# Optimization experiments

Measured on AMD Instinct MI355X. Metric: run time of the kernel, lower is better.

## Reference

```python
import jax, jax.numpy as jnp
import numpy as np

B, H, W, D, O = 16, 128, 128, 64, 256

def setup_inputs() -> dict:
    key = jax.random.key(0)
    k1, k2 = jax.random.split(key)
    x = jax.random.normal(k1, (B, H, W, D), dtype=jnp.float32)
    omega = jax.random.normal(k2, (O, D), dtype=jnp.float32)  # prototypes, init N(0,1)
    return {"x": x, "omega": omega}

def reference(x, omega):
    # Squared L2 distance from each pixel feature to each prototype,
    x2 = jnp.sum(x * x, axis=-1, keepdims=True)          # [B,H,W,1]
    p2 = jnp.sum(omega * omega, axis=-1)                  # [O]
    xp = jnp.einsum('bhwd,od->bhwo', x, omega)            # [B,H,W,O]
    dist = x2 + p2 - 2.0 * xp                             # [B,H,W,O]
    # original stacks per-prototype [B,H,W,1] slices along dim=3 -> [B,H,W,O,1]
    return dist[..., None]
```

## Files before the change

### kernel.cpp

```cpp
#include <hip/hip_runtime.h>


typedef __attribute__((ext_vector_type(4))) float f32x4;
typedef __attribute__((ext_vector_type(16))) float f32x16;
typedef __attribute__((ext_vector_type(8))) short s16x8;

constexpr int D_ = 64;
constexpr int O_ = 256;
constexpr int M_ = 16 * 128 * 128;
constexpr int ITERS = 8;
constexpr int PIX_PER_ITER = 32;
constexpr int PIX_PER_BLOCK = ITERS * PIX_PER_ITER;
constexpr int NBLOCKS = M_ / PIX_PER_BLOCK;
constexpr int LROW = 68;

__device__ __forceinline__ unsigned short f2bf(float f) {
    unsigned u = __builtin_bit_cast(unsigned, f);
    u += 0x7FFFu + ((u >> 16) & 1u);
    return (unsigned short)(u >> 16);
}

__global__ __launch_bounds__(256, 4) void dist_kernel(
    const float* __restrict__ x,
    const float* __restrict__ om,
    float* __restrict__ out)
{
    __shared__ float xstg[2][32 * LROW];

    const int tid  = threadIdx.x;
    const int wave = tid >> 6;
    const int lane = tid & 63;
    const int p    = lane & 31;
    const int h    = lane >> 5;

    s16x8 Bf[2][4];
    float p2r[2];
#pragma unroll
    for (int tt = 0; tt < 2; ++tt) {
        const int T = wave * 2 + tt;
        float p2p = 0.f;
#pragma unroll
        for (int s = 0; s < 4; ++s) {
            const float* src = om + (T * 32 + p) * D_ + s * 16 + h * 8;
            f32x4 v0 = *(const f32x4*)(src);
            f32x4 v1 = *(const f32x4*)(src + 4);
#pragma unroll
            for (int j = 0; j < 4; ++j) {
                Bf[tt][s][j]     = (short)f2bf(v0[j]); p2p += v0[j] * v0[j];
                Bf[tt][s][4 + j] = (short)f2bf(v1[j]); p2p += v1[j] * v1[j];
            }
        }
        p2p += __shfl_xor(p2p, 32);
        p2r[tt] = p2p;
    }

    const size_t gbase = (size_t)blockIdx.x * PIX_PER_BLOCK * D_;
    const int sr = tid >> 4;
    const int sc = (tid & 15) * 4;

    {
        const float* src = x + gbase + tid * 4;
        f32x4 v0 = __builtin_nontemporal_load((const f32x4*)(src));
        f32x4 v1 = __builtin_nontemporal_load((const f32x4*)(src + 1024));
        *(f32x4*)&xstg[0][sr * LROW + sc] = v0;
        *(f32x4*)&xstg[0][(16 + sr) * LROW + sc] = v1;
    }
    __syncthreads();

    for (int it = 0; it < ITERS; ++it) {
        const int cur = it & 1, nxt = cur ^ 1;
        const int rbase = blockIdx.x * PIX_PER_BLOCK + it * PIX_PER_ITER;

        f32x4 nv0, nv1;
        const bool pf = (it + 1 < ITERS);
        if (pf) {
            const float* src = x + gbase + (size_t)(it + 1) * (PIX_PER_ITER * D_) + tid * 4;
            nv0 = __builtin_nontemporal_load((const f32x4*)(src));
            nv1 = __builtin_nontemporal_load((const f32x4*)(src + 1024));
        }

        const float* row = &xstg[cur][p * LROW + h * 8];
        s16x8 Af[4];
        float x2p = 0.f;
#pragma unroll
        for (int s = 0; s < 4; ++s) {
            f32x4 a0 = *(const f32x4*)(row + s * 16);
            f32x4 a1 = *(const f32x4*)(row + s * 16 + 4);
#pragma unroll
            for (int j = 0; j < 4; ++j) {
                Af[s][j]     = (short)f2bf(a0[j]); x2p += a0[j] * a0[j];
                Af[s][4 + j] = (short)f2bf(a1[j]); x2p += a1[j] * a1[j];
            }
        }
        x2p += __shfl_xor(x2p, 32);

        float x2r[16];
#pragma unroll
        for (int reg = 0; reg < 16; ++reg)
            x2r[reg] = __shfl(x2p, (reg & 3) + 8 * (reg >> 2) + 4 * h);

#pragma unroll
        for (int tt = 0; tt < 2; ++tt) {
            const int T = wave * 2 + tt;
            f32x16 acc = {0.f, 0.f, 0.f, 0.f, 0.f, 0.f, 0.f, 0.f,
                          0.f, 0.f, 0.f, 0.f, 0.f, 0.f, 0.f, 0.f};
#pragma unroll
            for (int s = 0; s < 4; ++s)
                acc = __builtin_amdgcn_mfma_f32_32x32x16_bf16(Af[s], Bf[tt][s], acc, 0, 0, 0);

            float* const obase = out + (size_t)(rbase + 4 * h) * O_ + T * 32 + p;
#pragma unroll
            for (int reg = 0; reg < 16; ++reg) {
                const float val = (x2r[reg] + p2r[tt]) - 2.f * acc[reg];
                obase[((reg & 3) + 8 * (reg >> 2)) * O_] = val;
            }
        }

        if (pf) {
            *(f32x4*)&xstg[nxt][sr * LROW + sc] = nv0;
            *(f32x4*)&xstg[nxt][(16 + sr) * LROW + sc] = nv1;
        }
        __syncthreads();
    }
}

extern "C" void kernel_launch(void* const* d_in, const int* in_sizes, int n_in,
                              void* d_out, int out_size, void* d_ws, size_t ws_size,
                              hipStream_t stream) {
    const float* x  = (const float*)d_in[0];
    const float* om = (const float*)d_in[1];
    float* out = (float*)d_out;

    dist_kernel<<<dim3(NBLOCKS), dim3(256), 0, stream>>>(x, om, out);
}
```

Baseline: 69.53 us.

## Triple-buffer x staging with two-ahead prefetch and lightweight LDS barrier

Moves the x tile staging from a double buffer to a triple buffer, prefetching two iterations ahead into alternating register sets. It replaces __syncthreads with a barrier that waits only on LDS counters, so outstanding global stores and loads need not drain. The two MFMA chains are interleaved, and output stores are placed after the barrier so they overlap the next iteration. The cost is more registers and LDS, plus a fully unrolled loop, which may reduce occupancy.

```diff
diff --git a/kernel.cpp b/kernel.cpp
--- a/kernel.cpp
+++ b/kernel.cpp
@@ -20,12 +20,19 @@
     return (unsigned short)(u >> 16);
 }
 
+#define LDS_BARRIER() do {                                        \
+    asm volatile("s_waitcnt lgkmcnt(0)" ::: "memory");            \
+    __builtin_amdgcn_sched_barrier(0);                            \
+    __builtin_amdgcn_s_barrier();                                 \
+    __builtin_amdgcn_sched_barrier(0);                            \
+} while (0)
+
 __global__ __launch_bounds__(256, 4) void dist_kernel(
     const float* __restrict__ x,
     const float* __restrict__ om,
     float* __restrict__ out)
 {
-    __shared__ float xstg[2][32 * LROW];
+    __shared__ float xstg[3][32 * LROW];
 
     const int tid  = threadIdx.x;
     const int wave = tid >> 6;
@@ -33,8 +40,8 @@
     const int p    = lane & 31;
     const int h    = lane >> 5;
 
-    s16x8 Bf[2][4];
-    float p2r[2];
+    s16x8 Bf0[4], Bf1[4];
+    float p2r0 = 0.f, p2r1 = 0.f;
 #pragma unroll
     for (int tt = 0; tt < 2; ++tt) {
         const int T = wave * 2 + tt;
@@ -44,42 +51,51 @@
             const float* src = om + (T * 32 + p) * D_ + s * 16 + h * 8;
             f32x4 v0 = *(const f32x4*)(src);
             f32x4 v1 = *(const f32x4*)(src + 4);
+            s16x8 f;
 #pragma unroll
             for (int j = 0; j < 4; ++j) {
-                Bf[tt][s][j]     = (short)f2bf(v0[j]); p2p += v0[j] * v0[j];
-                Bf[tt][s][4 + j] = (short)f2bf(v1[j]); p2p += v1[j] * v1[j];
+                f[j]     = (short)f2bf(v0[j]); p2p += v0[j] * v0[j];
+                f[4 + j] = (short)f2bf(v1[j]); p2p += v1[j] * v1[j];
             }
+            if (tt == 0) Bf0[s] = f; else Bf1[s] = f;
         }
         p2p += __shfl_xor(p2p, 32);
-        p2r[tt] = p2p;
+        if (tt == 0) p2r0 = p2p; else p2r1 = p2p;
     }
 
     const size_t gbase = (size_t)blockIdx.x * PIX_PER_BLOCK * D_;
     const int sr = tid >> 4;
     const int sc = (tid & 15) * 4;
 
+    f32x4 nva0, nva1, nvb0, nvb1;
     {
-        const float* src = x + gbase + tid * 4;
-        f32x4 v0 = __builtin_nontemporal_load((const f32x4*)(src));
-        f32x4 v1 = __builtin_nontemporal_load((const f32x4*)(src + 1024));
-        *(f32x4*)&xstg[0][sr * LROW + sc] = v0;
-        *(f32x4*)&xstg[0][(16 + sr) * LROW + sc] = v1;
+        const float* s0 = x + gbase + tid * 4;
+        f32x4 t0 = __builtin_nontemporal_load((const f32x4*)(s0));
+        f32x4 t1 = __builtin_nontemporal_load((const f32x4*)(s0 + 1024));
+        const float* s1 = x + gbase + 2048 + tid * 4;
+        nvb0 = __builtin_nontemporal_load((const f32x4*)(s1));
+        nvb1 = __builtin_nontemporal_load((const f32x4*)(s1 + 1024));
+        *(f32x4*)&xstg[0][sr * LROW + sc] = t0;
+        *(f32x4*)&xstg[0][(16 + sr) * LROW + sc] = t1;
     }
     __syncthreads();
 
+#pragma unroll
     for (int it = 0; it < ITERS; ++it) {
-        const int cur = it & 1, nxt = cur ^ 1;
         const int rbase = blockIdx.x * PIX_PER_BLOCK + it * PIX_PER_ITER;
 
-        f32x4 nv0, nv1;
-        const bool pf = (it + 1 < ITERS);
-        if (pf) {
-            const float* src = x + gbase + (size_t)(it + 1) * (PIX_PER_ITER * D_) + tid * 4;
-            nv0 = __builtin_nontemporal_load((const f32x4*)(src));
-            nv1 = __builtin_nontemporal_load((const f32x4*)(src + 1024));
+        if (it + 2 < ITERS) {
+            const float* s = x + gbase + (size_t)(it + 2) * (PIX_PER_ITER * D_) + tid * 4;
+            if ((it & 1) == 0) {
+                nva0 = __builtin_nontemporal_load((const f32x4*)(s));
+                nva1 = __builtin_nontemporal_load((const f32x4*)(s + 1024));
+            } else {
+                nvb0 = __builtin_nontemporal_load((const f32x4*)(s));
+                nvb1 = __builtin_nontemporal_load((const f32x4*)(s + 1024));
+            }
         }
 
-        const float* row = &xstg[cur][p * LROW + h * 8];
+        const float* row = &xstg[it % 3][p * LROW + h * 8];
         s16x8 Af[4];
         float x2p = 0.f;
 #pragma unroll
@@ -94,33 +110,36 @@
         }
         x2p += __shfl_xor(x2p, 32);
 
-        float x2r[16];
+        f32x16 acc0 = {0.f, 0.f, 0.f, 0.f, 0.f, 0.f, 0.f, 0.f,
+                       0.f, 0.f, 0.f, 0.f, 0.f, 0.f, 0.f, 0.f};
+        f32x16 acc1 = acc0;
 #pragma unroll
-        for (int reg = 0; reg < 16; ++reg)
-            x2r[reg] = __shfl(x2p, (reg & 3) + 8 * (reg >> 2) + 4 * h);
-
-#pragma unroll
-        for (int tt = 0; tt < 2; ++tt) {
-            const int T = wave * 2 + tt;
-            f32x16 acc = {0.f, 0.f, 0.f, 0.f, 0.f, 0.f, 0.f, 0.f,
-                          0.f, 0.f, 0.f, 0.f, 0.f, 0.f, 0.f, 0.f};
-#pragma unroll
-            for (int s = 0; s < 4; ++s)
-                acc = __builtin_amdgcn_mfma_f32_32x32x16_bf16(Af[s], Bf[tt][s], acc, 0, 0, 0);
-
-            float* const obase = out + (size_t)(rbase + 4 * h) * O_ + T * 32 + p;
-#pragma unroll
-            for (int reg = 0; reg < 16; ++reg) {
-                const float val = (x2r[reg] + p2r[tt]) - 2.f * acc[reg];
-                obase[((reg & 3) + 8 * (reg >> 2)) * O_] = val;
-            }
+        for (int s = 0; s < 4; ++s) {
+            acc0 = __builtin_amdgcn_mfma_f32_32x32x16_bf16(Af[s], Bf0[s], acc0, 0, 0, 0);
+            acc1 = __builtin_amdgcn_mfma_f32_32x32x16_bf16(Af[s], Bf1[s], acc1, 0, 0, 0);
         }
 
-        if (pf) {
-            *(f32x4*)&xstg[nxt][sr * LROW + sc] = nv0;
-            *(f32x4*)&xstg[nxt][(16 + sr) * LROW + sc] = nv1;
+        if (it + 1 < ITERS) {
+            float* dst = &xstg[(it + 1) % 3][0];
+            if (((it + 1) & 1) == 0) {
+                *(f32x4*)&dst[sr * LROW + sc] = nva0;
+                *(f32x4*)&dst[(16 + sr) * LROW + sc] = nva1;
+            } else {
+                *(f32x4*)&dst[sr * LROW + sc] = nvb0;
+                *(f32x4*)&dst[(16 + sr) * LROW + sc] = nvb1;
+            }
+            LDS_BARRIER();
         }
-        __syncthreads();
+
+        const int T0 = wave * 2;
+        float* const ob0 = out + (size_t)(rbase + 4 * h) * O_ + T0 * 32 + p;
+#pragma unroll
+        for (int reg = 0; reg < 16; ++reg) {
+            const int r = (reg & 3) + 8 * (reg >> 2);
+            const float x2v = __shfl(x2p, r + 4 * h);
+            ob0[(size_t)r * O_]      = (x2v + p2r0) - 2.f * acc0[reg];
+            ob0[(size_t)r * O_ + 32] = (x2v + p2r1) - 2.f * acc1[reg];
+        }
     }
 }
 
```

Measured after the change: 67.60 us. -2.8%, faster.
